# Kernel optimization log

Hardware: AMD Instinct MI355X
Metric: run time of the kernel (lower is better)

The kernel has to match this reference:

```python
import jax, jax.numpy as jnp
import numpy as np

D_MODEL = 1024
H = 16
D_K = D_MODEL // H


def setup_inputs() -> dict:
    key = jax.random.key(0)
    ks = jax.random.split(key, 12)
    B, S = 4, 2048
    s = 1.0 / np.sqrt(D_MODEL)
    return {
        "Q": jax.random.normal(ks[0], (B, S, D_MODEL), jnp.float32),
        "K": jax.random.normal(ks[1], (B, S, D_MODEL), jnp.float32),
        "V": jax.random.normal(ks[2], (B, S, D_MODEL), jnp.float32),
        "attn_mask": jnp.ones((B, S), jnp.int32),
        "Wq": jax.random.normal(ks[3], (D_MODEL, D_MODEL), jnp.float32) * s,
        "bq": jax.random.normal(ks[4], (D_MODEL,), jnp.float32) * s,
        "Wk": jax.random.normal(ks[5], (D_MODEL, D_MODEL), jnp.float32) * s,
        "bk": jax.random.normal(ks[6], (D_MODEL,), jnp.float32) * s,
        "Wv": jax.random.normal(ks[7], (D_MODEL, D_MODEL), jnp.float32) * s,
        "bv": jax.random.normal(ks[8], (D_MODEL,), jnp.float32) * s,
        "Wo": jax.random.normal(ks[9], (D_MODEL, D_MODEL), jnp.float32) * s,
        "bo": jax.random.normal(ks[10], (D_MODEL,), jnp.float32) * s,
    }


def _split_heads(x):
    B, S, _ = x.shape
    return x.reshape(B, S, H, D_K).transpose(0, 2, 1, 3)  # (B,H,S,Dk)


def reference(Q, K, V, attn_mask, Wq, bq, Wk, bk, Wv, bv, Wo, bo):
    # Linear projections (torch Linear: x @ W.T + b)
    q = _split_heads(Q @ Wq.T + bq)
    k = _split_heads(K @ Wk.T + bk)
    v = _split_heads(V @ Wv.T + bv)
    scale = 1.0 / jnp.sqrt(jnp.asarray(D_K, q.dtype))
    scores = jnp.einsum("bhqd,bhkd->bhqk", q, k) * scale  # (B,H,S,S)
    # 2-D mask (B,S) broadcast over heads and query positions; 0 -> -inf
    mask = attn_mask[:, None, None, :]
    scores = jnp.where(mask == 0, -jnp.inf, scores)
    attn = jax.nn.softmax(scores, axis=-1)
    # dropout_proba = 0.0 -> identity
    x = jnp.einsum("bhqk,bhkd->bhqd", attn, v)
    B, _, S, _ = x.shape
    x = x.transpose(0, 2, 1, 3).reshape(B, S, D_MODEL)
    return x @ Wo.T + bo
```

## Files before the change

### kernel.cpp

```cpp
#include <hip/hip_runtime.h>
#include <stdint.h>

typedef unsigned short u16;
typedef __attribute__((ext_vector_type(8))) unsigned short u16x8;
typedef __attribute__((ext_vector_type(4))) unsigned short u16x4;
typedef __attribute__((ext_vector_type(2))) __fp16 h16x2;
typedef __attribute__((ext_vector_type(4))) _Float16 f16x4;
typedef __attribute__((ext_vector_type(8))) _Float16 f16x8;
typedef __attribute__((ext_vector_type(4))) float f32x4;

#define MFMA16F16(a,b,c)  __builtin_amdgcn_mfma_f32_16x16x16f16((a),(b),(c),0,0,0)
#define MFMA32F16(a,b,c)  __builtin_amdgcn_mfma_f32_16x16x32_f16((a),(b),(c),0,0,0)

__device__ __forceinline__ f32x4 f4zero() {
    f32x4 z; z[0]=0.f; z[1]=0.f; z[2]=0.f; z[3]=0.f; return z;
}
__device__ __forceinline__ u16x8 cvth8(float4 a, float4 b) {
    union { h16x2 h[4]; u16x8 u; } U;
    U.h[0] = __builtin_amdgcn_cvt_pkrtz(a.x, a.y);
    U.h[1] = __builtin_amdgcn_cvt_pkrtz(a.z, a.w);
    U.h[2] = __builtin_amdgcn_cvt_pkrtz(b.x, b.y);
    U.h[3] = __builtin_amdgcn_cvt_pkrtz(b.z, b.w);
    return U.u;
}

#define GLDS(gp, lp) __builtin_amdgcn_global_load_lds( \
    (const __attribute__((address_space(1))) void*)(gp), \
    (__attribute__((address_space(3))) void*)(lp), 16, 0, 0)

#define QSC 0.1803368801111601f

__global__ __launch_bounds__(256) void conv_w(
    const float* __restrict__ w0, const float* __restrict__ w1,
    const float* __restrict__ w2, const float* __restrict__ w3,
    u16* __restrict__ out)
{
    const int t = blockIdx.x >> 8;
    const float* src = (t == 0) ? w0 : (t == 1) ? w1 : (t == 2) ? w2 : w3;
    const size_t idx = (size_t)(blockIdx.x & 255) * 4096 + (size_t)threadIdx.x * 16;
    u16* dst = out + (size_t)t * 1048576 + idx;
    float4 a0 = *(const float4*)(src + idx);
    float4 a1 = *(const float4*)(src + idx + 4);
    float4 a2 = *(const float4*)(src + idx + 8);
    float4 a3 = *(const float4*)(src + idx + 12);
    *(u16x8*)dst       = cvth8(a0, a1);
    *(u16x8*)(dst + 8) = cvth8(a2, a3);
}

__global__ __launch_bounds__(256) void conv_x(
    const float* __restrict__ x0, const float* __restrict__ x1,
    const float* __restrict__ x2, u16* __restrict__ out)
{
    const int t = blockIdx.y;
    const float* src = (t == 0) ? x0 : (t == 1) ? x1 : x2;
    const size_t idx = (size_t)blockIdx.x * 4096 + (size_t)threadIdx.x * 16;
    u16* dst = out + (size_t)t * 8388608 + idx;
    float4 a0 = *(const float4*)(src + idx);
    float4 a1 = *(const float4*)(src + idx + 4);
    float4 a2 = *(const float4*)(src + idx + 8);
    float4 a3 = *(const float4*)(src + idx + 12);
    *(u16x8*)dst       = cvth8(a0, a1);
    *(u16x8*)(dst + 8) = cvth8(a2, a3);
}

template<int MODE>
__global__ __launch_bounds__(256, 2) void gemm_qkv(
    const float* __restrict__ Qf, const float* __restrict__ Kf, const float* __restrict__ Vf,
    const u16* __restrict__ xc, const u16* __restrict__ wc,
    const float* __restrict__ Wqf, const float* __restrict__ Wkf, const float* __restrict__ Wvf,
    const float* __restrict__ bq, const float* __restrict__ bk, const float* __restrict__ bv,
    u16* __restrict__ qhp, u16* __restrict__ khp, u16* __restrict__ vtp)
{
    __shared__ __align__(16) char smem[34816];
    u16* As = (u16*)smem;
    u16* Bs = As + 4096;
    u16* Ct = (u16*)smem;

    const int t  = blockIdx.y >> 3;
    const int n0 = (blockIdx.y & 7) * 128;
    const int m0 = blockIdx.x * 128;
    const float* X    = (t == 0) ? Qf : (t == 1) ? Kf : Vf;
    const float* Wf   = (t == 0) ? Wqf : (t == 1) ? Wkf : Wvf;
    const float* bias = (t == 0) ? bq : (t == 1) ? bk : bv;
    const u16*   Wb   = wc + (size_t)t * 1048576;
    const u16*   Xc   = xc + (size_t)t * 8388608;
    u16*         dst  = (t == 0) ? qhp : (t == 1) ? khp : vtp;
    const float  scl  = (t == 0) ? QSC : 1.0f;

    const int tid  = threadIdx.x;
    const int wave = tid >> 6, lane = tid & 63;
    const int quad = lane >> 4, l16 = lane & 15;
    const int wm = (wave >> 1) * 64, wn = (wave & 1) * 64;

    const int c0 = wave, c1 = wave + 4;
    const size_t gl = (size_t)(lane >> 2) * 1024 + (lane & 3) * 8;
    const int sr = tid >> 1, hh = tid & 1;
    const size_t xrow = (size_t)(m0 + sr) * 1024 + hh * 16;
    const size_t wrow = (size_t)(n0 + sr) * 1024 + hh * 16;

    f32x4 acc[4][4];
    for (int i = 0; i < 4; i++) for (int j = 0; j < 4; j++) acc[i][j] = f4zero();

    for (int k0 = 0; k0 < 1024; k0 += 32) {
        if (MODE == 2) {
            GLDS(Xc + (size_t)(m0 + c0 * 16) * 1024 + gl + k0, As + c0 * 512);
            GLDS(Xc + (size_t)(m0 + c1 * 16) * 1024 + gl + k0, As + c1 * 512);
        } else {
            float4 a0 = *(const float4*)(X + xrow + k0);
            float4 a1 = *(const float4*)(X + xrow + k0 + 4);
            float4 a2 = *(const float4*)(X + xrow + k0 + 8);
            float4 a3 = *(const float4*)(X + xrow + k0 + 12);
            *(u16x8*)(As + sr * 32 + hh * 16)     = cvth8(a0, a1);
            *(u16x8*)(As + sr * 32 + hh * 16 + 8) = cvth8(a2, a3);
        }
        if (MODE >= 1) {
            GLDS(Wb + (size_t)(n0 + c0 * 16) * 1024 + gl + k0, Bs + c0 * 512);
            GLDS(Wb + (size_t)(n0 + c1 * 16) * 1024 + gl + k0, Bs + c1 * 512);
        } else {
            float4 b0 = *(const float4*)(Wf + wrow + k0);
            float4 b1 = *(const float4*)(Wf + wrow + k0 + 4);
            float4 b2 = *(const float4*)(Wf + wrow + k0 + 8);
            float4 b3 = *(const float4*)(Wf + wrow + k0 + 12);
            *(u16x8*)(Bs + sr * 32 + hh * 16)     = cvth8(b0, b1);
            *(u16x8*)(Bs + sr * 32 + hh * 16 + 8) = cvth8(b2, b3);
        }
        __syncthreads();

        f16x8 af[4], bfr[4];
#pragma unroll
        for (int i = 0; i < 4; i++) {
            af[i]  = *(const f16x8*)(As + (wm + i * 16 + l16) * 32 + quad * 8);
            bfr[i] = *(const f16x8*)(Bs + (wn + i * 16 + l16) * 32 + quad * 8);
        }
#pragma unroll
        for (int i = 0; i < 4; i++)
#pragma unroll
            for (int j = 0; j < 4; j++)
                acc[i][j] = MFMA32F16(af[i], bfr[j], acc[i][j]);
        __syncthreads();
    }

#pragma unroll
    for (int i = 0; i < 4; i++) {
        const int row = wm + i * 16 + quad * 4;
#pragma unroll
        for (int j = 0; j < 4; j++) {
            const int col = wn + j * 16 + l16;
            const float bv2 = bias[n0 + col];
#pragma unroll
            for (int r = 0; r < 2; r++) {
                union { h16x2 h; unsigned u; } P;
                P.h = __builtin_amdgcn_cvt_pkrtz((acc[i][j][2*r] + bv2) * scl,
                                                 (acc[i][j][2*r+1] + bv2) * scl);
                Ct[(row + 2*r)     * 136 + col] = (u16)(P.u & 0xFFFF);
                Ct[(row + 2*r + 1) * 136 + col] = (u16)(P.u >> 16);
            }
        }
    }
    __syncthreads();

    if (t < 2) {
        const int row = tid >> 1, half = tid & 1;
        const int m = m0 + row, b = m >> 11, s = m & 2047;
        const int h = (n0 >> 6) + half;
        u16* o = dst + ((size_t)(b * 16 + h) * 2048 + s) * 64;
        const u16* src = Ct + row * 136 + half * 64;
#pragma unroll
        for (int j = 0; j < 64; j += 8) *(u16x8*)(o + j) = *(const u16x8*)(src + j);
    } else {
        const int col = tid >> 1, shalf = tid & 1;
        const int h = (n0 >> 6) + (col >> 6), d = col & 63;
        const int mb = m0 + shalf * 64, b = mb >> 11, sb = mb & 2047;
        u16* o = dst + (size_t)((b * 16 + h) * 64 + d) * 2048 + sb;
#pragma unroll
        for (int j0 = 0; j0 < 64; j0 += 8) {
            u16x8 tv;
#pragma unroll
            for (int j = 0; j < 8; j++) tv[j] = Ct[(shalf * 64 + j0 + j) * 136 + col];
            *(u16x8*)(o + j0) = tv;
        }
    }
}

template<bool WGLDS>
__global__ __launch_bounds__(256, 2) void gemm_o(
    const u16* __restrict__ Xb, const u16* __restrict__ wcO,
    const float* __restrict__ Wf, const float* __restrict__ bias,
    float* __restrict__ out)
{
    __shared__ __align__(16) u16 As[4096];
    __shared__ __align__(16) u16 Bs[4096];

    const int tid  = threadIdx.x;
    const int wave = tid >> 6, lane = tid & 63;
    const int quad = lane >> 4, l16 = lane & 15;
    const int m0 = blockIdx.x * 128, n0 = blockIdx.y * 128;
    const int wm = (wave >> 1) * 64, wn = (wave & 1) * 64;

    const int c0 = wave, c1 = wave + 4;
    const size_t gl = (size_t)(lane >> 2) * 1024 + (lane & 3) * 8;
    const int sr = tid >> 1, hh = tid & 1;
    const size_t wrow = (size_t)(n0 + sr) * 1024 + hh * 16;

    f32x4 acc[4][4];
    for (int i = 0; i < 4; i++) for (int j = 0; j < 4; j++) acc[i][j] = f4zero();

    for (int k0 = 0; k0 < 1024; k0 += 32) {
        GLDS(Xb + (size_t)(m0 + c0 * 16) * 1024 + gl + k0, As + c0 * 512);
        GLDS(Xb + (size_t)(m0 + c1 * 16) * 1024 + gl + k0, As + c1 * 512);
        if (WGLDS) {
            GLDS(wcO + (size_t)(n0 + c0 * 16) * 1024 + gl + k0, Bs + c0 * 512);
            GLDS(wcO + (size_t)(n0 + c1 * 16) * 1024 + gl + k0, Bs + c1 * 512);
        } else {
            float4 b0 = *(const float4*)(Wf + wrow + k0);
            float4 b1 = *(const float4*)(Wf + wrow + k0 + 4);
            float4 b2 = *(const float4*)(Wf + wrow + k0 + 8);
            float4 b3 = *(const float4*)(Wf + wrow + k0 + 12);
            *(u16x8*)(Bs + sr * 32 + hh * 16)     = cvth8(b0, b1);
            *(u16x8*)(Bs + sr * 32 + hh * 16 + 8) = cvth8(b2, b3);
        }
        __syncthreads();

        f16x8 af[4], bfr[4];
#pragma unroll
        for (int i = 0; i < 4; i++) {
            af[i]  = *(const f16x8*)(As + (wm + i * 16 + l16) * 32 + quad * 8);
            bfr[i] = *(const f16x8*)(Bs + (wn + i * 16 + l16) * 32 + quad * 8);
        }
#pragma unroll
        for (int i = 0; i < 4; i++)
#pragma unroll
            for (int j = 0; j < 4; j++)
                acc[i][j] = MFMA32F16(af[i], bfr[j], acc[i][j]);
        __syncthreads();
    }

#pragma unroll
    for (int i = 0; i < 4; i++)
#pragma unroll
        for (int j = 0; j < 4; j++) {
            const int col = wn + j * 16 + l16;
            const float bv = bias[n0 + col];
#pragma unroll
            for (int r = 0; r < 4; r++)
                out[(size_t)(m0 + wm + i * 16 + quad * 4 + r) * 1024 + n0 + col] = acc[i][j][r] + bv;
        }
}

__global__ __launch_bounds__(256, 4) void attn_fused(
    const u16* __restrict__ qh, const u16* __restrict__ kh,
    const u16* __restrict__ vth, const int* __restrict__ mask,
    u16* __restrict__ xout)
{
    __shared__ __align__(16) u16 Ksh[64 * 72];
    __shared__ __align__(16) u16 Vsh[64 * 68];
    __shared__ float mshf[64];

    const int tid = threadIdx.x, wave = tid >> 6, lane = tid & 63;
    const int quad = lane >> 4, l16 = lane & 15;
    const int bh = blockIdx.y, b = bh >> 4, h = bh & 15;
    const int wq = blockIdx.x * 128 + wave * 32;

    f16x8 qf[2][2];
#pragma unroll
    for (int qg = 0; qg < 2; qg++)
#pragma unroll
        for (int kc = 0; kc < 2; kc++)
            qf[qg][kc] = *(const f16x8*)(qh + ((size_t)bh * 2048 + wq + qg * 16 + l16) * 64
                                         + kc * 32 + quad * 8);

    f32x4 o[2][4];
#pragma unroll
    for (int qg = 0; qg < 2; qg++)
        for (int dt = 0; dt < 4; dt++) o[qg][dt] = f4zero();
    f32x4 lacc[2]; lacc[0] = f4zero(); lacc[1] = f4zero();
    f16x4 ones;
    ones[0] = (_Float16)1.f; ones[1] = (_Float16)1.f;
    ones[2] = (_Float16)1.f; ones[3] = (_Float16)1.f;

    const int skey = tid >> 2, sc = (tid & 3) * 16;
    const u16* kg = kh  + ((size_t)bh * 2048 + skey) * 64 + sc;
    const u16* vg = vth + ((size_t)bh * 64 + skey) * 2048 + sc;

    for (int kk = 0; kk < 2048; kk += 64) {
        *(u16x8*)(Ksh + skey * 72 + sc)     = *(const u16x8*)(kg + (size_t)kk * 64);
        *(u16x8*)(Ksh + skey * 72 + sc + 8) = *(const u16x8*)(kg + (size_t)kk * 64 + 8);
        {
            const u16x8 v0 = *(const u16x8*)(vg + kk);
            const u16x8 v1 = *(const u16x8*)(vg + kk + 8);
            u16* vd = Vsh + skey * 68 + sc;
            *(u16x4*)(vd)      = (u16x4){v0[0], v0[1], v0[2], v0[3]};
            *(u16x4*)(vd + 4)  = (u16x4){v0[4], v0[5], v0[6], v0[7]};
            *(u16x4*)(vd + 8)  = (u16x4){v1[0], v1[1], v1[2], v1[3]};
            *(u16x4*)(vd + 12) = (u16x4){v1[4], v1[5], v1[6], v1[7]};
        }
        if (tid < 64) mshf[tid] = mask[b * 2048 + kk + tid] ? -10.0f : -1.0e30f;
        __syncthreads();

#pragma unroll
        for (int nt = 0; nt < 4; nt++) {
            const f16x8 kf0 = *(const f16x8*)(Ksh + (nt * 16 + l16) * 72 + quad * 8);
            const f16x8 kf1 = *(const f16x8*)(Ksh + (nt * 16 + l16) * 72 + 32 + quad * 8);
            const float4 mb = *(const float4*)(mshf + nt * 16 + quad * 4);
            f16x4 pf[2];
#pragma unroll
            for (int qg = 0; qg < 2; qg++) {
                f32x4 z;
                z[0] = mb.x; z[1] = mb.y; z[2] = mb.z; z[3] = mb.w;
                z = MFMA32F16(kf0, qf[qg][0], z);
                z = MFMA32F16(kf1, qf[qg][1], z);
                union { h16x2 h[2]; f16x4 v; } U;
                U.h[0] = __builtin_amdgcn_cvt_pkrtz(__builtin_amdgcn_exp2f(z[0]),
                                                    __builtin_amdgcn_exp2f(z[1]));
                U.h[1] = __builtin_amdgcn_cvt_pkrtz(__builtin_amdgcn_exp2f(z[2]),
                                                    __builtin_amdgcn_exp2f(z[3]));
                pf[qg] = U.v;
            }
            lacc[0] = MFMA16F16(ones, pf[0], lacc[0]);
            lacc[1] = MFMA16F16(ones, pf[1], lacc[1]);
#pragma unroll
            for (int dt = 0; dt < 4; dt++) {
                const f16x4 vf = *(const f16x4*)(Vsh + (dt * 16 + l16) * 68 + nt * 16 + quad * 4);
                o[0][dt] = MFMA16F16(vf, pf[0], o[0][dt]);
                o[1][dt] = MFMA16F16(vf, pf[1], o[1][dt]);
            }
        }
        __syncthreads();
    }

#pragma unroll
    for (int qg = 0; qg < 2; qg++) {
        const float inv = 1.0f / lacc[qg][0];
        const int row = wq + qg * 16 + l16;
        u16* op = xout + ((size_t)b * 2048 + row) * 1024 + h * 64;
#pragma unroll
        for (int dt = 0; dt < 4; dt++) {
            union { h16x2 h[2]; u16x4 u; } U;
            U.h[0] = __builtin_amdgcn_cvt_pkrtz(o[qg][dt][0] * inv, o[qg][dt][1] * inv);
            U.h[1] = __builtin_amdgcn_cvt_pkrtz(o[qg][dt][2] * inv, o[qg][dt][3] * inv);
            *(u16x4*)(op + dt * 16 + quad * 4) = U.u;
        }
    }
}

extern "C" void kernel_launch(void* const* d_in, const int* in_sizes, int n_in,
                              void* d_out, int out_size, void* d_ws, size_t ws_size,
                              hipStream_t stream)
{
    const float* Q   = (const float*)d_in[0];
    const float* K   = (const float*)d_in[1];
    const float* V   = (const float*)d_in[2];
    const int*   msk = (const int*)d_in[3];
    const float* Wq  = (const float*)d_in[4];
    const float* bq  = (const float*)d_in[5];
    const float* Wk  = (const float*)d_in[6];
    const float* bk  = (const float*)d_in[7];
    const float* Wv  = (const float*)d_in[8];
    const float* bv  = (const float*)d_in[9];
    const float* Wo  = (const float*)d_in[10];
    const float* bo  = (const float*)d_in[11];

    u16* base = (u16*)d_ws;
    dim3 blk(256);
    dim3 gq(64, 24);
    dim3 ga(16, 64);
    dim3 go(64, 8);

    if (ws_size >= 125829120UL) {
        u16* wc  = base;
        u16* xc  = base + 4194304;
        u16* qhp = xc + 25165824;
        u16* khp = qhp + 8388608;
        u16* vtp = khp + 8388608;
        u16* xs  = vtp + 8388608;
        conv_w<<<1024, blk, 0, stream>>>(Wq, Wk, Wv, Wo, wc);
        conv_x<<<dim3(2048, 3), blk, 0, stream>>>(Q, K, V, xc);
        gemm_qkv<2><<<gq, blk, 0, stream>>>(Q, K, V, xc, wc,
            nullptr, nullptr, nullptr, bq, bk, bv, qhp, khp, vtp);
        attn_fused<<<ga, blk, 0, stream>>>(qhp, khp, vtp, msk, xs);
        gemm_o<true><<<go, blk, 0, stream>>>(xs, wc + 3 * 1048576, nullptr, bo, (float*)d_out);
    } else if (ws_size >= ((size_t)72 << 20)) {
        u16* wc  = base;
        u16* qhp = base + 4194304;
        u16* khp = qhp + 8388608;
        u16* vtp = khp + 8388608;
        u16* xs  = vtp + 8388608;
        conv_w<<<1024, blk, 0, stream>>>(Wq, Wk, Wv, Wo, wc);
        gemm_qkv<1><<<gq, blk, 0, stream>>>(Q, K, V, nullptr, wc,
            nullptr, nullptr, nullptr, bq, bk, bv, qhp, khp, vtp);
        attn_fused<<<ga, blk, 0, stream>>>(qhp, khp, vtp, msk, xs);
        gemm_o<true><<<go, blk, 0, stream>>>(xs, wc + 3 * 1048576, nullptr, bo, (float*)d_out);
    } else {
        u16* qhp = base;
        u16* khp = qhp + 8388608;
        u16* vtp = khp + 8388608;
        u16* xs  = vtp + 8388608;
        gemm_qkv<0><<<gq, blk, 0, stream>>>(Q, K, V, nullptr, nullptr,
            Wq, Wk, Wv, bq, bk, bv, qhp, khp, vtp);
        attn_fused<<<ga, blk, 0, stream>>>(qhp, khp, vtp, msk, xs);
        gemm_o<false><<<go, blk, 0, stream>>>(xs, nullptr, Wo, bo, (float*)d_out);
    }
}
```

Measured before the change: 360.2 us.

## Double-buffer attention K/V tiles with async LDS loads and swizzled layout

The attention kernel now double-buffers K, V and mask tiles in shared memory. The next K tile is prefetched via global-to-LDS loads into an XOR-swizzled layout, and the next V tile is held in registers while the current tile is computed under raised wave priority. Blocks are remapped so neighbouring blocks share the same head, and the GEMM launch bounds rise to 3 blocks per CU. The workspace threshold drops because the attention output now reuses the converted-input buffer. This roughly doubles attention LDS use and adds register pressure, which may reduce occupancy.

```diff
diff --git a/kernel.cpp b/kernel.cpp
--- a/kernel.cpp
+++ b/kernel.cpp
@@ -64,7 +64,7 @@
 }
 
 template<int MODE>
-__global__ __launch_bounds__(256, 2) void gemm_qkv(
+__global__ __launch_bounds__(256, 3) void gemm_qkv(
     const float* __restrict__ Qf, const float* __restrict__ Kf, const float* __restrict__ Vf,
     const u16* __restrict__ xc, const u16* __restrict__ wc,
     const float* __restrict__ Wqf, const float* __restrict__ Wkf, const float* __restrict__ Wvf,
@@ -183,7 +183,7 @@
 }
 
 template<bool WGLDS>
-__global__ __launch_bounds__(256, 2) void gemm_o(
+__global__ __launch_bounds__(256, 3) void gemm_o(
     const u16* __restrict__ Xb, const u16* __restrict__ wcO,
     const float* __restrict__ Wf, const float* __restrict__ bias,
     float* __restrict__ out)
@@ -252,14 +252,18 @@
     const u16* __restrict__ vth, const int* __restrict__ mask,
     u16* __restrict__ xout)
 {
-    __shared__ __align__(16) u16 Ksh[64 * 72];
-    __shared__ __align__(16) u16 Vsh[64 * 68];
-    __shared__ float mshf[64];
+    __shared__ __align__(16) u16 Ksh[2][4096];
+    __shared__ __align__(16) u16 Vsh[2][4352];
+    __shared__ float mshf[2][64];
 
     const int tid = threadIdx.x, wave = tid >> 6, lane = tid & 63;
     const int quad = lane >> 4, l16 = lane & 15;
-    const int bh = blockIdx.y, b = bh >> 4, h = bh & 15;
-    const int wq = blockIdx.x * 128 + wave * 32;
+
+    const int flat = blockIdx.x + (blockIdx.y << 4);
+    const int xr = flat & 7, xc_ = flat >> 3;
+    const int qb = xc_ & 15, bh = xr + ((xc_ >> 4) << 3);
+    const int b = bh >> 4, h = bh & 15;
+    const int wq = qb * 128 + wave * 32;
 
     f16x8 qf[2][2];
 #pragma unroll
@@ -278,30 +282,52 @@
     ones[0] = (_Float16)1.f; ones[1] = (_Float16)1.f;
     ones[2] = (_Float16)1.f; ones[3] = (_Float16)1.f;
 
+    const int klr = lane >> 3;
+    const size_t kgoff = (size_t)((lane & 7) ^ klr) << 3;
+    const u16* kgb = kh + (size_t)bh * 2048 * 64;
+
     const int skey = tid >> 2, sc = (tid & 3) * 16;
-    const u16* kg = kh  + ((size_t)bh * 2048 + skey) * 64 + sc;
     const u16* vg = vth + ((size_t)bh * 64 + skey) * 2048 + sc;
-
-    for (int kk = 0; kk < 2048; kk += 64) {
-        *(u16x8*)(Ksh + skey * 72 + sc)     = *(const u16x8*)(kg + (size_t)kk * 64);
-        *(u16x8*)(Ksh + skey * 72 + sc + 8) = *(const u16x8*)(kg + (size_t)kk * 64 + 8);
-        {
-            const u16x8 v0 = *(const u16x8*)(vg + kk);
-            const u16x8 v1 = *(const u16x8*)(vg + kk + 8);
-            u16* vd = Vsh + skey * 68 + sc;
-            *(u16x4*)(vd)      = (u16x4){v0[0], v0[1], v0[2], v0[3]};
-            *(u16x4*)(vd + 4)  = (u16x4){v0[4], v0[5], v0[6], v0[7]};
-            *(u16x4*)(vd + 8)  = (u16x4){v1[0], v1[1], v1[2], v1[3]};
-            *(u16x4*)(vd + 12) = (u16x4){v1[4], v1[5], v1[6], v1[7]};
-        }
-        if (tid < 64) mshf[tid] = mask[b * 2048 + kk + tid] ? -10.0f : -1.0e30f;
-        __syncthreads();
-
+    const int mrow = b * 2048;
+
+    {
+        GLDS(kgb + (size_t)(wave * 16 + klr) * 64 + kgoff,     &Ksh[0][wave * 1024]);
+        GLDS(kgb + (size_t)(wave * 16 + 8 + klr) * 64 + kgoff, &Ksh[0][wave * 1024 + 512]);
+        const u16x8 v0 = *(const u16x8*)(vg);
+        const u16x8 v1 = *(const u16x8*)(vg + 8);
+        u16* vd = &Vsh[0][skey * 68 + sc];
+        *(u16x4*)(vd)      = (u16x4){v0[0], v0[1], v0[2], v0[3]};
+        *(u16x4*)(vd + 4)  = (u16x4){v0[4], v0[5], v0[6], v0[7]};
+        *(u16x4*)(vd + 8)  = (u16x4){v1[0], v1[1], v1[2], v1[3]};
+        *(u16x4*)(vd + 12) = (u16x4){v1[4], v1[5], v1[6], v1[7]};
+        if (tid < 64) mshf[0][tid] = mask[mrow + tid] ? -10.0f : -1.0e30f;
+    }
+    __syncthreads();
+
+    for (int t = 0; t < 32; ++t) {
+        const int cur = t & 1;
+        const u16* Kc = &Ksh[cur][0];
+        const u16* Vc = &Vsh[cur][0];
+
+        u16x8 v0, v1; int mreg = 1;
+        const int kk2 = (t + 1) * 64;
+        if (t < 31) {
+            GLDS(kgb + (size_t)(kk2 + wave * 16 + klr) * 64 + kgoff,
+                 &Ksh[cur ^ 1][wave * 1024]);
+            GLDS(kgb + (size_t)(kk2 + wave * 16 + 8 + klr) * 64 + kgoff,
+                 &Ksh[cur ^ 1][wave * 1024 + 512]);
+            v0 = *(const u16x8*)(vg + kk2);
+            v1 = *(const u16x8*)(vg + kk2 + 8);
+            if (tid < 64) mreg = mask[mrow + kk2 + tid];
+        }
+
+        __builtin_amdgcn_s_setprio(1);
 #pragma unroll
         for (int nt = 0; nt < 4; nt++) {
-            const f16x8 kf0 = *(const f16x8*)(Ksh + (nt * 16 + l16) * 72 + quad * 8);
-            const f16x8 kf1 = *(const f16x8*)(Ksh + (nt * 16 + l16) * 72 + 32 + quad * 8);
-            const float4 mb = *(const float4*)(mshf + nt * 16 + quad * 4);
+            const int kro = (nt * 16 + l16) * 64;
+            const f16x8 kf0 = *(const f16x8*)(Kc + kro + ((quad ^ (l16 & 7)) << 3));
+            const f16x8 kf1 = *(const f16x8*)(Kc + kro + (((quad ^ 4) ^ (l16 & 7)) << 3));
+            const float4 mb = *(const float4*)(&mshf[cur][nt * 16 + quad * 4]);
             f16x4 pf[2];
 #pragma unroll
             for (int qg = 0; qg < 2; qg++) {
@@ -320,10 +346,20 @@
             lacc[1] = MFMA16F16(ones, pf[1], lacc[1]);
 #pragma unroll
             for (int dt = 0; dt < 4; dt++) {
-                const f16x4 vf = *(const f16x4*)(Vsh + (dt * 16 + l16) * 68 + nt * 16 + quad * 4);
+                const f16x4 vf = *(const f16x4*)(Vc + (dt * 16 + l16) * 68 + nt * 16 + quad * 4);
                 o[0][dt] = MFMA16F16(vf, pf[0], o[0][dt]);
                 o[1][dt] = MFMA16F16(vf, pf[1], o[1][dt]);
             }
+        }
+        __builtin_amdgcn_s_setprio(0);
+
+        if (t < 31) {
+            u16* vd = &Vsh[cur ^ 1][skey * 68 + sc];
+            *(u16x4*)(vd)      = (u16x4){v0[0], v0[1], v0[2], v0[3]};
+            *(u16x4*)(vd + 4)  = (u16x4){v0[4], v0[5], v0[6], v0[7]};
+            *(u16x4*)(vd + 8)  = (u16x4){v1[0], v1[1], v1[2], v1[3]};
+            *(u16x4*)(vd + 12) = (u16x4){v1[4], v1[5], v1[6], v1[7]};
+            if (tid < 64) mshf[cur ^ 1][tid] = mreg ? -10.0f : -1.0e30f;
         }
         __syncthreads();
     }
@@ -366,13 +402,13 @@
     dim3 ga(16, 64);
     dim3 go(64, 8);
 
-    if (ws_size >= 125829120UL) {
+    if (ws_size >= 109051904UL) {
         u16* wc  = base;
         u16* xc  = base + 4194304;
         u16* qhp = xc + 25165824;
         u16* khp = qhp + 8388608;
         u16* vtp = khp + 8388608;
-        u16* xs  = vtp + 8388608;
+        u16* xs  = xc;
         conv_w<<<1024, blk, 0, stream>>>(Wq, Wk, Wv, Wo, wc);
         conv_x<<<dim3(2048, 3), blk, 0, stream>>>(Q, K, V, xc);
         gemm_qkv<2><<<gq, blk, 0, stream>>>(Q, K, V, xc, wc,
```

Measured after the change: 354.4 us. About the same (-1.6%).
